# Kernel optimization log

Measured on AMD Instinct MI355X. Metric: run time of the kernel, lower is better.

Reference implementation:

```python
import jax, jax.numpy as jnp
import numpy as np

EMBED = 1024
HIDDEN = 1024

def setup_inputs() -> dict:
    key = jax.random.key(0)
    k1, k2, k3, k4, k5 = jax.random.split(key, 5)
    B, T = 32, 512
    s_ih = 1.0 / np.sqrt(HIDDEN)
    x = jax.random.normal(k1, (B, T, EMBED), dtype=jnp.float32)
    # PyTorch nn.RNN params: W_ih [H,E], W_hh [H,H], b_ih [H], b_hh [H], init U(-1/sqrt(H), 1/sqrt(H))
    W_ih = jax.random.uniform(k2, (HIDDEN, EMBED), minval=-s_ih, maxval=s_ih, dtype=jnp.float32)
    W_hh = jax.random.uniform(k3, (HIDDEN, HIDDEN), minval=-s_ih, maxval=s_ih, dtype=jnp.float32)
    b_ih = jax.random.uniform(k4, (HIDDEN,), minval=-s_ih, maxval=s_ih, dtype=jnp.float32)
    b_hh = jax.random.uniform(k5, (HIDDEN,), minval=-s_ih, maxval=s_ih, dtype=jnp.float32)
    return {"x": x, "W_ih": W_ih, "W_hh": W_hh, "b_ih": b_ih, "b_hh": b_hh}

def reference(x, W_ih, W_hh, b_ih, b_hh):
    # h_t = tanh(x_t @ W_ih^T + b_ih + h_{t-1} @ W_hh^T + b_hh), h_0 = 0
    B, T, E = x.shape
    H = W_hh.shape[0]
    # Precompute the input projection for all timesteps in one big GEMM.
    xp = jnp.einsum('bte,he->bth', x, W_ih) + (b_ih + b_hh)  # [B,T,H]
    h0 = jnp.zeros((B, H), dtype=x.dtype)

    def step(h, xp_t):
        h_new = jnp.tanh(xp_t + h @ W_hh.T)
        return h_new, h_new

    _, outs = jax.lax.scan(step, h0, jnp.swapaxes(xp, 0, 1))  # outs: [T,B,H]
    return jnp.swapaxes(outs, 0, 1)  # [B,T,H]
```

## Files before the change

kernel.cpp:

```cpp
#include <hip/hip_runtime.h>
#include <stdint.h>

#define B_ 32
#define T_ 512
#define E_ 1024
#define H_ 1024
#define NWAVE 64

typedef __attribute__((ext_vector_type(8))) short short8;
typedef __attribute__((ext_vector_type(4))) float floatx4;
typedef __attribute__((ext_vector_type(4))) int int4v;
typedef unsigned long long ull;

union U16 { ull u[2]; short8 s; int4v v; };

__device__ __forceinline__ unsigned short bf16_of(float f) {
    unsigned u = __float_as_uint(f);
    return (unsigned short)((u + 0x8000u) >> 16);
}

__device__ __forceinline__ short8 load_bf8(const float* __restrict__ p) {
    const float4* q = (const float4*)p;
    float4 v0 = q[0];
    float4 v1 = q[1];
    short8 r;
    r[0] = (short)bf16_of(v0.x); r[1] = (short)bf16_of(v0.y);
    r[2] = (short)bf16_of(v0.z); r[3] = (short)bf16_of(v0.w);
    r[4] = (short)bf16_of(v1.x); r[5] = (short)bf16_of(v1.y);
    r[6] = (short)bf16_of(v1.z); r[7] = (short)bf16_of(v1.w);
    return r;
}

__global__ __launch_bounds__(256) void k_xp(const float* __restrict__ x,
                                            const float* __restrict__ Wih,
                                            const float* __restrict__ bih,
                                            const float* __restrict__ bhh,
                                            float* __restrict__ out) {
    const int tid  = threadIdx.x;
    const int w    = tid >> 6;
    const int lane = tid & 63;
    const int l15  = lane & 15;
    const int quad = lane >> 4;
    const int rb = blockIdx.x & 127;
    const int cb = blockIdx.x >> 7;
    const int row_base = rb * 128 + w * 32;
    const int col_base = cb * 128;

    floatx4 acc[2][8];
#pragma unroll
    for (int i = 0; i < 2; i++)
#pragma unroll
        for (int j = 0; j < 8; j++) acc[i][j] = (floatx4)0.0f;

    for (int k0 = 0; k0 < E_; k0 += 32) {
        const int koff = k0 + quad * 8;
        short8 a[2];
#pragma unroll
        for (int mt = 0; mt < 2; mt++)
            a[mt] = load_bf8(x + (size_t)(row_base + mt * 16 + l15) * E_ + koff);
        short8 b[8];
#pragma unroll
        for (int nt = 0; nt < 8; nt++)
            b[nt] = load_bf8(Wih + (size_t)(col_base + nt * 16 + l15) * E_ + koff);
#pragma unroll
        for (int mt = 0; mt < 2; mt++)
#pragma unroll
            for (int nt = 0; nt < 8; nt++)
                acc[mt][nt] = __builtin_amdgcn_mfma_f32_16x16x32_bf16(
                    a[mt], b[nt], acc[mt][nt], 0, 0, 0);
    }

#pragma unroll
    for (int nt = 0; nt < 8; nt++) {
        const int col = col_base + nt * 16 + l15;
        const float bias = bih[col] + bhh[col];
#pragma unroll
        for (int mt = 0; mt < 2; mt++) {
            const int row = row_base + mt * 16 + quad * 4;
#pragma unroll
            for (int r = 0; r < 4; r++)
                out[(size_t)(row + r) * H_ + col] = acc[mt][nt][r] + bias;
        }
    }
}

__global__ void k_init(unsigned* __restrict__ ws, int ring) {
    const int i = blockIdx.x * blockDim.x + threadIdx.x;
    if (i < 1024) ws[i] = 0u;
    ws[1024 + (ring - 1) * 16384 + i] = 0u;
}

__global__ __launch_bounds__(64, 1) void k_rnn(const float* __restrict__ Whh,
                                               float* __restrict__ out,
                                               unsigned* __restrict__ ws,
                                               int ring) {
    const int lane = threadIdx.x;
    const int l15  = lane & 15;
    const int quad = lane >> 4;
    const int wid  = blockIdx.x;
    const int j0   = wid * 16;

    unsigned* flags = ws;

    const int mt_s = lane >> 5;
    const int sub  = (lane >> 4) & 1;
    const int m_s  = lane & 15;
    const int slot = (wid >> 1) * 128 + mt_s * 64 + (wid & 1) * 32 + sub * 16 + m_s;
    const int lds_off = mt_s * 512 + m_s * 32 + sub * 16;

    __shared__ unsigned short sh[512];

    short8 wreg[32];
#pragma unroll
    for (int c = 0; c < 32; c++)
        wreg[c] = load_bf8(Whh + (size_t)(j0 + l15) * H_ + c * 32 + quad * 8);

#pragma unroll 1
    for (int t = 0; t < T_; t++) {
        const int rs = (t + ring - 1) & (ring - 1);
        const int wsl = t & (ring - 1);
        const ull* hA = (const ull*)(ws + 1024 + rs * 16384);
        const ull* hB = hA + 4096;
        ull* nxA = (ull*)(ws + 1024 + wsl * 16384);
        ull* nxB = nxA + 4096;

        float xv[2][4];
#pragma unroll
        for (int mt = 0; mt < 2; mt++)
#pragma unroll
            for (int r = 0; r < 4; r++) {
                const int b = mt * 16 + quad * 4 + r;
                xv[mt][r] = out[((size_t)b * T_ + t) * H_ + j0 + l15];
            }

        if (t > 0) {
            const unsigned tv = (unsigned)t;
            while (true) {
                unsigned v = __hip_atomic_load(&flags[lane * 16], __ATOMIC_RELAXED,
                                               __HIP_MEMORY_SCOPE_AGENT);
                if (__ballot(v < tv) == 0ull) break;
            }
            if ((t & (ring - 1)) == 0)
                __builtin_amdgcn_fence(__ATOMIC_ACQUIRE, "agent");
            else
                asm volatile("" ::: "memory");
        }

        floatx4 acc[2];
        acc[0] = (floatx4)0.0f;
        acc[1] = (floatx4)0.0f;
#pragma unroll
        for (int c = 0; c < 32; c++) {
#pragma unroll
            for (int mt = 0; mt < 2; mt++) {
                U16 u;
                u.u[0] = hA[(c * 2 + mt) * 64 + lane];
                u.u[1] = hB[(c * 2 + mt) * 64 + lane];
                acc[mt] = __builtin_amdgcn_mfma_f32_16x16x32_bf16(u.s, wreg[c],
                                                                  acc[mt], 0, 0, 0);
            }
        }

        float hv[2][4];
#pragma unroll
        for (int mt = 0; mt < 2; mt++)
#pragma unroll
            for (int r = 0; r < 4; r++) {
                const float p = xv[mt][r] + acc[mt][r];
                const float h = 1.0f - 2.0f / (__expf(2.0f * p) + 1.0f);
                hv[mt][r] = h;
                sh[(mt * 16 + quad * 4 + r) * 16 + l15] = bf16_of(h);
            }

        U16 pk;
        pk.v = *(const int4v*)((const char*)sh + lds_off);
        __hip_atomic_store(nxA + slot, pk.u[0], __ATOMIC_RELAXED,
                           __HIP_MEMORY_SCOPE_AGENT);
        __hip_atomic_store(nxB + slot, pk.u[1], __ATOMIC_RELAXED,
                           __HIP_MEMORY_SCOPE_AGENT);

        asm volatile("s_waitcnt vmcnt(0)" ::: "memory");
        if (lane == 0)
            __hip_atomic_store(&flags[wid * 16], (unsigned)(t + 1),
                               __ATOMIC_RELAXED, __HIP_MEMORY_SCOPE_AGENT);

#pragma unroll
        for (int mt = 0; mt < 2; mt++)
#pragma unroll
            for (int r = 0; r < 4; r++) {
                const int b = mt * 16 + quad * 4 + r;
                out[((size_t)b * T_ + t) * H_ + j0 + l15] = hv[mt][r];
            }
    }
}

extern "C" void kernel_launch(void* const* d_in, const int* in_sizes, int n_in,
                              void* d_out, int out_size, void* d_ws, size_t ws_size,
                              hipStream_t stream) {
    const float* x   = (const float*)d_in[0];
    const float* Wih = (const float*)d_in[1];
    const float* Whh = (const float*)d_in[2];
    const float* bih = (const float*)d_in[3];
    const float* bhh = (const float*)d_in[4];
    float* out = (float*)d_out;
    unsigned* ws = (unsigned*)d_ws;

    const size_t need8 = (size_t)(1024 + 8 * 16384) * sizeof(unsigned);
    const int ring = (ws_size >= need8) ? 8 : 2;

    k_init<<<64, 256, 0, stream>>>(ws, ring);
    k_xp<<<128 * 8, 256, 0, stream>>>(x, Wih, bih, bhh, out);
    k_rnn<<<NWAVE, 64, 0, stream>>>(Whh, out, ws, ring);
}
```

Before: 2.800 ms.

## Add helper wave to prefetch input projections and write outputs off the critical path

The recurrent kernel now runs two waves per block. The compute wave keeps the MFMA recurrence and the cross-block flag sync. The helper wave prefetches the next timestep's projected inputs into double-buffered LDS and writes the previous step's hidden states to global memory with nontemporal stores. This moves global load and store latency off the serial per-step critical path, at the cost of one block barrier per step. The input-projection GEMM's block index mapping is also reordered so that consecutive blocks share a row tile.

```diff
diff --git a/kernel.cpp b/kernel.cpp
--- a/kernel.cpp
+++ b/kernel.cpp
@@ -41,8 +41,8 @@
     const int lane = tid & 63;
     const int l15  = lane & 15;
     const int quad = lane >> 4;
-    const int rb = blockIdx.x & 127;
-    const int cb = blockIdx.x >> 7;
+    const int rb = blockIdx.x >> 3;
+    const int cb = blockIdx.x & 7;
     const int row_base = rb * 128 + w * 32;
     const int col_base = cb * 128;
 
@@ -90,107 +90,143 @@
     ws[1024 + (ring - 1) * 16384 + i] = 0u;
 }
 
-__global__ __launch_bounds__(64, 1) void k_rnn(const float* __restrict__ Whh,
-                                               float* __restrict__ out,
-                                               unsigned* __restrict__ ws,
-                                               int ring) {
-    const int lane = threadIdx.x;
-    const int l15  = lane & 15;
-    const int quad = lane >> 4;
+__global__ __launch_bounds__(128, 1) void k_rnn(const float* __restrict__ Whh,
+                                                float* __restrict__ out,
+                                                unsigned* __restrict__ ws,
+                                                int ring) {
+    const int tid  = threadIdx.x;
+    const int wv   = tid >> 6;
+    const int lane = tid & 63;
     const int wid  = blockIdx.x;
     const int j0   = wid * 16;
 
     unsigned* flags = ws;
 
-    const int mt_s = lane >> 5;
-    const int sub  = (lane >> 4) & 1;
-    const int m_s  = lane & 15;
-    const int slot = (wid >> 1) * 128 + mt_s * 64 + (wid & 1) * 32 + sub * 16 + m_s;
-    const int lds_off = mt_s * 512 + m_s * 32 + sub * 16;
-
-    __shared__ unsigned short sh[512];
-
-    short8 wreg[32];
-#pragma unroll
-    for (int c = 0; c < 32; c++)
-        wreg[c] = load_bf8(Whh + (size_t)(j0 + l15) * H_ + c * 32 + quad * 8);
+    __shared__ unsigned short sh_h[512];
+    __shared__ float sh_hf[2][512];
+    __shared__ float sh_xp[2][512];
+
+    if (wv == 0) {
+        const int l15  = lane & 15;
+        const int quad = lane >> 4;
+        const int mt_s = lane >> 5;
+        const int sub  = (lane >> 4) & 1;
+        const int m_s  = lane & 15;
+        const int slot = (wid >> 1) * 128 + mt_s * 64 + (wid & 1) * 32 + sub * 16 + m_s;
+        const int lds_off = mt_s * 512 + m_s * 32 + sub * 16;
+
+        short8 wreg[32];
+#pragma unroll
+        for (int c = 0; c < 32; c++)
+            wreg[c] = load_bf8(Whh + (size_t)(j0 + l15) * H_ + c * 32 + quad * 8);
+
+        __syncthreads();
 
 #pragma unroll 1
-    for (int t = 0; t < T_; t++) {
-        const int rs = (t + ring - 1) & (ring - 1);
-        const int wsl = t & (ring - 1);
-        const ull* hA = (const ull*)(ws + 1024 + rs * 16384);
-        const ull* hB = hA + 4096;
-        ull* nxA = (ull*)(ws + 1024 + wsl * 16384);
-        ull* nxB = nxA + 4096;
-
-        float xv[2][4];
-#pragma unroll
-        for (int mt = 0; mt < 2; mt++)
-#pragma unroll
-            for (int r = 0; r < 4; r++) {
-                const int b = mt * 16 + quad * 4 + r;
-                xv[mt][r] = out[((size_t)b * T_ + t) * H_ + j0 + l15];
-            }
-
-        if (t > 0) {
-            const unsigned tv = (unsigned)t;
-            while (true) {
-                unsigned v = __hip_atomic_load(&flags[lane * 16], __ATOMIC_RELAXED,
-                                               __HIP_MEMORY_SCOPE_AGENT);
-                if (__ballot(v < tv) == 0ull) break;
-            }
-            if ((t & (ring - 1)) == 0)
-                __builtin_amdgcn_fence(__ATOMIC_ACQUIRE, "agent");
-            else
-                asm volatile("" ::: "memory");
-        }
-
-        floatx4 acc[2];
-        acc[0] = (floatx4)0.0f;
-        acc[1] = (floatx4)0.0f;
-#pragma unroll
-        for (int c = 0; c < 32; c++) {
-#pragma unroll
-            for (int mt = 0; mt < 2; mt++) {
-                U16 u;
-                u.u[0] = hA[(c * 2 + mt) * 64 + lane];
-                u.u[1] = hB[(c * 2 + mt) * 64 + lane];
-                acc[mt] = __builtin_amdgcn_mfma_f32_16x16x32_bf16(u.s, wreg[c],
-                                                                  acc[mt], 0, 0, 0);
-            }
-        }
-
-        float hv[2][4];
-#pragma unroll
-        for (int mt = 0; mt < 2; mt++)
-#pragma unroll
-            for (int r = 0; r < 4; r++) {
-                const float p = xv[mt][r] + acc[mt][r];
-                const float h = 1.0f - 2.0f / (__expf(2.0f * p) + 1.0f);
-                hv[mt][r] = h;
-                sh[(mt * 16 + quad * 4 + r) * 16 + l15] = bf16_of(h);
-            }
-
-        U16 pk;
-        pk.v = *(const int4v*)((const char*)sh + lds_off);
-        __hip_atomic_store(nxA + slot, pk.u[0], __ATOMIC_RELAXED,
-                           __HIP_MEMORY_SCOPE_AGENT);
-        __hip_atomic_store(nxB + slot, pk.u[1], __ATOMIC_RELAXED,
-                           __HIP_MEMORY_SCOPE_AGENT);
-
-        asm volatile("s_waitcnt vmcnt(0)" ::: "memory");
-        if (lane == 0)
-            __hip_atomic_store(&flags[wid * 16], (unsigned)(t + 1),
-                               __ATOMIC_RELAXED, __HIP_MEMORY_SCOPE_AGENT);
-
-#pragma unroll
-        for (int mt = 0; mt < 2; mt++)
-#pragma unroll
-            for (int r = 0; r < 4; r++) {
-                const int b = mt * 16 + quad * 4 + r;
-                out[((size_t)b * T_ + t) * H_ + j0 + l15] = hv[mt][r];
-            }
+        for (int t = 0; t < T_; t++) {
+            const int rs  = (t + ring - 1) & (ring - 1);
+            const int wsl = t & (ring - 1);
+            const ull* hA = (const ull*)(ws + 1024 + rs * 16384);
+            const ull* hB = hA + 4096;
+            ull* nxA = (ull*)(ws + 1024 + wsl * 16384);
+            ull* nxB = nxA + 4096;
+
+            if (t > 0) {
+                const unsigned tv = (unsigned)t;
+                while (true) {
+                    unsigned v = __hip_atomic_load(&flags[lane * 16],
+                                                   __ATOMIC_RELAXED,
+                                                   __HIP_MEMORY_SCOPE_AGENT);
+                    if (__ballot(v < tv) == 0ull) break;
+                }
+                if ((t & (ring - 1)) == 0)
+                    __builtin_amdgcn_fence(__ATOMIC_ACQUIRE, "agent");
+                else
+                    asm volatile("" ::: "memory");
+            }
+
+            floatx4 acc[2];
+            acc[0] = (floatx4)0.0f;
+            acc[1] = (floatx4)0.0f;
+#pragma unroll
+            for (int c = 0; c < 32; c++) {
+#pragma unroll
+                for (int mt = 0; mt < 2; mt++) {
+                    U16 u;
+                    u.u[0] = hA[(c * 2 + mt) * 64 + lane];
+                    u.u[1] = hB[(c * 2 + mt) * 64 + lane];
+                    acc[mt] = __builtin_amdgcn_mfma_f32_16x16x32_bf16(
+                        u.s, wreg[c], acc[mt], 0, 0, 0);
+                }
+            }
+
+#pragma unroll
+            for (int mt = 0; mt < 2; mt++)
+#pragma unroll
+                for (int r = 0; r < 4; r++) {
+                    const int b = mt * 16 + quad * 4 + r;
+                    const float p = sh_xp[t & 1][b * 16 + l15] + acc[mt][r];
+                    const float h = 1.0f - 2.0f / (__expf(2.0f * p) + 1.0f);
+                    sh_hf[t & 1][b * 16 + l15] = h;
+                    sh_h[b * 16 + l15] = bf16_of(h);
+                }
+
+            U16 pk;
+            pk.v = *(const int4v*)((const char*)sh_h + lds_off);
+            __hip_atomic_store(nxA + slot, pk.u[0], __ATOMIC_RELAXED,
+                               __HIP_MEMORY_SCOPE_AGENT);
+            __hip_atomic_store(nxB + slot, pk.u[1], __ATOMIC_RELAXED,
+                               __HIP_MEMORY_SCOPE_AGENT);
+
+            asm volatile("s_waitcnt vmcnt(0)" ::: "memory");
+            if (lane == 0)
+                __hip_atomic_store(&flags[wid * 16], (unsigned)(t + 1),
+                                   __ATOMIC_RELAXED, __HIP_MEMORY_SCOPE_AGENT);
+
+            __syncthreads();
+        }
+    } else {
+        const int b  = lane >> 1;
+        const int cs = (lane & 1) * 8;
+        const float* xp_base = out + (size_t)b * T_ * H_ + j0 + cs;
+        float*       out_base = out + (size_t)b * T_ * H_ + j0 + cs;
+
+        {
+            float4 v0 = *(const float4*)(xp_base + 0);
+            float4 v1 = *(const float4*)(xp_base + 4);
+            *(float4*)&sh_xp[0][b * 16 + cs]     = v0;
+            *(float4*)&sh_xp[0][b * 16 + cs + 4] = v1;
+        }
+        __syncthreads();
+
+        float hold[8];
+#pragma unroll 1
+        for (int t = 0; t < T_; t++) {
+            float4 v0, v1;
+            const bool more = (t + 1 < T_);
+            if (more) {
+                v0 = *(const float4*)(xp_base + (size_t)(t + 1) * H_);
+                v1 = *(const float4*)(xp_base + (size_t)(t + 1) * H_ + 4);
+            }
+            if (t > 0) {
+#pragma unroll
+                for (int k = 0; k < 8; k++)
+                    __builtin_nontemporal_store(
+                        hold[k], out_base + (size_t)(t - 1) * H_ + k);
+            }
+            if (more) {
+                *(float4*)&sh_xp[(t + 1) & 1][b * 16 + cs]     = v0;
+                *(float4*)&sh_xp[(t + 1) & 1][b * 16 + cs + 4] = v1;
+            }
+            __syncthreads();
+#pragma unroll
+            for (int k = 0; k < 8; k++)
+                hold[k] = sh_hf[t & 1][b * 16 + cs + k];
+        }
+#pragma unroll
+        for (int k = 0; k < 8; k++)
+            __builtin_nontemporal_store(hold[k],
+                                        out_base + (size_t)(T_ - 1) * H_ + k);
     }
 }
 
@@ -210,5 +246,5 @@
 
     k_init<<<64, 256, 0, stream>>>(ws, ring);
     k_xp<<<128 * 8, 256, 0, stream>>>(x, Wih, bih, bhh, out);
-    k_rnn<<<NWAVE, 64, 0, stream>>>(Whh, out, ws, ring);
-}
+    k_rnn<<<NWAVE, 128, 0, stream>>>(Whh, out, ws, ring);
+}
```

Result: faster. 2.588 ms (-7.6%).
